# Kernel optimization log

Measured on AMD Instinct MI355X. Metric: run time of the kernel, lower is better.

The kernel has to match this reference:

```python
import jax, jax.numpy as jnp
import numpy as np

B = 4096   # batch (samples)
V = 64     # num_vars
H = 512    # hidden_dim


def setup_inputs() -> dict:
    key = jax.random.key(0)
    k0, k1, k2, k3 = jax.random.split(key, 4)
    x = jax.random.normal(k0, (B, V), dtype=jnp.float32)
    # learned params: adjacency logits + stacked per-variable 2-layer MLPs
    adj_weights = jax.random.normal(k1, (V, V), dtype=jnp.float32) * 0.1
    W1 = jax.random.normal(k2, (V, V - 1, H), dtype=jnp.float32) * (1.0 / np.sqrt(V - 1))
    b1 = jnp.zeros((V, H), dtype=jnp.float32)
    W2 = jax.random.normal(k3, (V, H), dtype=jnp.float32) * (1.0 / np.sqrt(H))
    b2 = jnp.zeros((V,), dtype=jnp.float32)
    return {"x": x, "adj_weights": adj_weights, "W1": W1, "b1": b1, "W2": W2, "b2": b2}


def reference(x, adj_weights, W1, b1, W2, b2):
    Vn = adj_weights.shape[0]
    # sigmoid adjacency with zeroed diagonal
    adj = jax.nn.sigmoid(adj_weights) * (1.0 - jnp.eye(Vn, dtype=adj_weights.dtype))
    # idx[i, j] = j if j < i else j + 1  -> columns of x excluding variable i
    j = jnp.arange(Vn - 1)
    idx = j[None, :] + (j[None, :] >= jnp.arange(Vn)[:, None])  # [V, V-1] int
    gathered = x[:, idx]                                  # [B, V, V-1]
    w = jnp.take_along_axis(adj, idx, axis=1)             # [V, V-1] (row i, cols != i)
    weighted = gathered * w[None, :, :]                   # [B, V, V-1]
    # batched small MLP per variable
    h = jax.nn.relu(jnp.einsum('bvk,vkh->bvh', weighted, W1) + b1[None])  # [B, V, H]
    out = jnp.einsum('bvh,vh->bv', h, W2) + b2[None]                      # [B, V]
    return out
```

## Files before the change

### kernel.cpp

```cpp
#include <hip/hip_runtime.h>
#include <hip/hip_bf16.h>

constexpr int Bn = 4096;
constexpr int Vn = 64;
constexpr int Hn = 512;

typedef __attribute__((ext_vector_type(8))) short bf16x8;
typedef __attribute__((ext_vector_type(4))) float f32x4;
typedef __attribute__((ext_vector_type(8))) unsigned short u16x8;
typedef __attribute__((ext_vector_type(4))) _Float16 f16x4;

__device__ __forceinline__ unsigned short f2bf(float f) {
    union { float f; unsigned int u; } x; x.f = f;
    unsigned int u = x.u;
    u += 0x7fffu + ((u >> 16) & 1u);
    return (unsigned short)(u >> 16);
}

__global__ void prep_all(const float* __restrict__ adjw,
                         const float* __restrict__ W1,
                         const float* __restrict__ x,
                         unsigned short* __restrict__ bfrag,
                         unsigned short* __restrict__ afrag) {
    if (blockIdx.x < 1024) {
        int nb   = (blockIdx.x & 7) * 128 + (blockIdx.x >> 3);
        int tid  = nb * 256 + threadIdx.x;
        int lane = tid & 63;
        int ks   = (tid >> 6) & 1;
        int nt   = (tid >> 7) & 31;
        int v    = tid >> 12;

        int n     = nt * 16 + (lane & 15);
        int kbase = ks * 32 + ((lane >> 4) << 3);

        u16x8 o;
#pragma unroll
        for (int e = 0; e < 8; ++e) {
            int k = kbase + e;
            float val = 0.f;
            if (k != v) {
                float aw = adjw[v * Vn + k];
                float s  = 1.f / (1.f + __expf(-aw));
                int  j   = k - (k > v);
                val = s * W1[((size_t)(v * (Vn - 1) + j)) * Hn + n];
            }
            o[e] = f2bf(val);
        }
        *reinterpret_cast<u16x8*>(bfrag + (size_t)tid * 8) = o;
    } else {
        int tid  = (blockIdx.x - 1024) * 256 + threadIdx.x;
        int lane = tid & 63;
        int ks   = (tid >> 6) & 1;
        int mt   = tid >> 7;

        int b     = mt * 16 + (lane & 15);
        int kbase = ks * 32 + ((lane >> 4) << 3);

        u16x8 o;
#pragma unroll
        for (int e = 0; e < 8; ++e)
            o[e] = f2bf(x[(size_t)b * Vn + kbase + e]);
        *reinterpret_cast<u16x8*>(afrag + (size_t)tid * 8) = o;
    }
}

__global__ __launch_bounds__(512, 4)
void main_k(const unsigned short* __restrict__ afrag,
            const unsigned short* __restrict__ bfrag,
            const float* __restrict__ b1, const float* __restrict__ W2,
            const float* __restrict__ b2, float* __restrict__ out) {
    __shared__ __align__(16) unsigned char smem[2 * 16384 + 512 * 9 * 4];

    int t    = threadIdx.x;
    int wid  = t >> 6;
    int lane = t & 63;
    int xcd  = blockIdx.x & 7;
    int idx  = blockIdx.x >> 3;
    int v    = xcd * 8 + (idx & 7);
    int ro   = idx >> 3;

    int hi4  = (lane >> 4) << 2;

    const unsigned short* wpan = bfrag + (size_t)v * 32768;
    bf16x8 Wf[4][2];
#pragma unroll
    for (int j = 0; j < 4; ++j)
#pragma unroll
        for (int ks = 0; ks < 2; ++ks)
            Wf[j][ks] = *reinterpret_cast<const bf16x8*>(
                wpan + ((size_t)((wid * 4 + j) * 2 + ks)) * 512 + lane * 8);

    f32x4 b1bc[4];
    f16x4 w2A[4];
#pragma unroll
    for (int j = 0; j < 4; ++j) {
        int ntg = wid * 4 + j;
        b1bc[j] = *reinterpret_cast<const f32x4*>(b1 + v * Hn + ntg * 16 + hi4);
        f32x4 wv = *reinterpret_cast<const f32x4*>(W2 + v * Hn + ntg * 16 + hi4);
#pragma unroll
        for (int e = 0; e < 4; ++e) w2A[j][e] = (_Float16)wv[e];
    }

    const unsigned char* asrc = reinterpret_cast<const unsigned char*>(afrag)
                              + (size_t)ro * 65536;
    {
        u16x8 s0 = *reinterpret_cast<const u16x8*>(asrc + t * 16);
        u16x8 s1 = *reinterpret_cast<const u16x8*>(asrc + 8192 + t * 16);
        *reinterpret_cast<u16x8*>(smem + t * 16) = s0;
        *reinterpret_cast<u16x8*>(smem + 8192 + t * 16) = s1;
    }
    __syncthreads();

    float* partials = reinterpret_cast<float*>(smem + 32768);

#pragma unroll
    for (int c = 0; c < 4; ++c) {
        u16x8 s0, s1;
        if (c < 3) {
            s0 = *reinterpret_cast<const u16x8*>(asrc + (c + 1) * 16384 + t * 16);
            s1 = *reinterpret_cast<const u16x8*>(asrc + (c + 1) * 16384 + 8192 + t * 16);
        }

        const unsigned char* lb = smem + (c & 1) * 16384;
#pragma unroll
        for (int mt = 0; mt < 8; ++mt) {
            bf16x8 a0 = *reinterpret_cast<const bf16x8*>(lb + ((mt * 2 + 0) * 64 + lane) * 16);
            bf16x8 a1 = *reinterpret_cast<const bf16x8*>(lb + ((mt * 2 + 1) * 64 + lane) * 16);
            f32x4 acc = {0.f, 0.f, 0.f, 0.f};
#pragma unroll
            for (int j = 0; j < 4; ++j) {
                f32x4 c1 = __builtin_amdgcn_mfma_f32_16x16x32_bf16(Wf[j][0], a0, b1bc[j], 0, 0, 0);
                c1 = __builtin_amdgcn_mfma_f32_16x16x32_bf16(Wf[j][1], a1, c1, 0, 0, 0);
                f16x4 hb;
#pragma unroll
                for (int e = 0; e < 4; ++e)
                    hb[e] = (_Float16)fmaxf(c1[e], 0.f);
                acc = __builtin_amdgcn_mfma_f32_16x16x16f16(w2A[j], hb, acc, 0, 0, 0);
            }
            if (lane < 16)
                partials[(c * 128 + mt * 16 + lane) * 9 + wid] = acc[0];
        }

        if (c < 3) {
            unsigned char* nbuf = smem + ((c + 1) & 1) * 16384;
            *reinterpret_cast<u16x8*>(nbuf + t * 16) = s0;
            *reinterpret_cast<u16x8*>(nbuf + 8192 + t * 16) = s1;
        }
        __syncthreads();
    }

    float s = b2[v];
#pragma unroll
    for (int w = 0; w < 8; ++w) s += partials[t * 9 + w];
    out[(size_t)(ro * 512 + t) * Vn + v] = s;
}

extern "C" void kernel_launch(void* const* d_in, const int* in_sizes, int n_in,
                              void* d_out, int out_size, void* d_ws, size_t ws_size,
                              hipStream_t stream) {
    const float* x    = (const float*)d_in[0];
    const float* adjw = (const float*)d_in[1];
    const float* W1   = (const float*)d_in[2];
    const float* b1   = (const float*)d_in[3];
    const float* W2   = (const float*)d_in[4];
    const float* b2   = (const float*)d_in[5];
    float* out = (float*)d_out;

    unsigned short* bfrag = (unsigned short*)d_ws;
    unsigned short* afrag = bfrag + (size_t)Vn * Vn * Hn;

    prep_all<<<1152, 256, 0, stream>>>(adjw, W1, x, bfrag, afrag);
    main_k<<<512, 512, 0, stream>>>(afrag, bfrag, b1, W2, b2, out);
}
```

Measured before the change: 30.22 us.

## Fuse weight and input bf16 prep into main kernel, drop prep launch

```diff
diff --git a/kernel.cpp b/kernel.cpp
--- a/kernel.cpp
+++ b/kernel.cpp
@@ -10,6 +10,8 @@
 typedef __attribute__((ext_vector_type(8))) unsigned short u16x8;
 typedef __attribute__((ext_vector_type(4))) _Float16 f16x4;
 
+union bfcast { u16x8 u; bf16x8 b; };
+
 __device__ __forceinline__ unsigned short f2bf(float f) {
     union { float f; unsigned int u; } x; x.f = f;
     unsigned int u = x.u;
@@ -17,79 +19,42 @@
     return (unsigned short)(u >> 16);
 }
 
-__global__ void prep_all(const float* __restrict__ adjw,
-                         const float* __restrict__ W1,
-                         const float* __restrict__ x,
-                         unsigned short* __restrict__ bfrag,
-                         unsigned short* __restrict__ afrag) {
-    if (blockIdx.x < 1024) {
-        int nb   = (blockIdx.x & 7) * 128 + (blockIdx.x >> 3);
-        int tid  = nb * 256 + threadIdx.x;
-        int lane = tid & 63;
-        int ks   = (tid >> 6) & 1;
-        int nt   = (tid >> 7) & 31;
-        int v    = tid >> 12;
-
-        int n     = nt * 16 + (lane & 15);
-        int kbase = ks * 32 + ((lane >> 4) << 3);
-
-        u16x8 o;
-#pragma unroll
-        for (int e = 0; e < 8; ++e) {
-            int k = kbase + e;
-            float val = 0.f;
-            if (k != v) {
-                float aw = adjw[v * Vn + k];
-                float s  = 1.f / (1.f + __expf(-aw));
-                int  j   = k - (k > v);
-                val = s * W1[((size_t)(v * (Vn - 1) + j)) * Hn + n];
-            }
-            o[e] = f2bf(val);
-        }
-        *reinterpret_cast<u16x8*>(bfrag + (size_t)tid * 8) = o;
-    } else {
-        int tid  = (blockIdx.x - 1024) * 256 + threadIdx.x;
-        int lane = tid & 63;
-        int ks   = (tid >> 6) & 1;
-        int mt   = tid >> 7;
-
-        int b     = mt * 16 + (lane & 15);
-        int kbase = ks * 32 + ((lane >> 4) << 3);
-
-        u16x8 o;
-#pragma unroll
-        for (int e = 0; e < 8; ++e)
-            o[e] = f2bf(x[(size_t)b * Vn + kbase + e]);
-        *reinterpret_cast<u16x8*>(afrag + (size_t)tid * 8) = o;
-    }
-}
-
 __global__ __launch_bounds__(512, 4)
-void main_k(const unsigned short* __restrict__ afrag,
-            const unsigned short* __restrict__ bfrag,
+void main_k(const float* __restrict__ x,
+            const float* __restrict__ adjw,
+            const float* __restrict__ W1,
             const float* __restrict__ b1, const float* __restrict__ W2,
             const float* __restrict__ b2, float* __restrict__ out) {
-    __shared__ __align__(16) unsigned char smem[2 * 16384 + 512 * 9 * 4];
+    __shared__ __align__(16) unsigned char smem[2 * 16384 + 512 * 9 * 4 + 256];
+    float* partials = reinterpret_cast<float*>(smem + 2 * 16384);
+    float* sig      = reinterpret_cast<float*>(smem + 2 * 16384 + 512 * 9 * 4);
 
     int t    = threadIdx.x;
     int wid  = t >> 6;
     int lane = t & 63;
-    int xcd  = blockIdx.x & 7;
-    int idx  = blockIdx.x >> 3;
-    int v    = xcd * 8 + (idx & 7);
-    int ro   = idx >> 3;
+    int v    = (blockIdx.x & 7) * 8 + ((blockIdx.x >> 3) & 7);
+    int ro   = blockIdx.x >> 6;
 
-    int hi4  = (lane >> 4) << 2;
+    if (t < 64) {
+        float aw = adjw[v * Vn + t];
+        sig[t] = (t == v) ? 0.f : 1.f / (1.f + __expf(-aw));
+    }
 
-    const unsigned short* wpan = bfrag + (size_t)v * 32768;
-    bf16x8 Wf[4][2];
-#pragma unroll
-    for (int j = 0; j < 4; ++j)
-#pragma unroll
-        for (int ks = 0; ks < 2; ++ks)
-            Wf[j][ks] = *reinterpret_cast<const bf16x8*>(
-                wpan + ((size_t)((wid * 4 + j) * 2 + ks)) * 512 + lane * 8);
+    int s_mt  = t >> 7;
+    int s_ks  = (t >> 6) & 1;
+    int s_kb  = s_ks * 32 + ((lane >> 4) << 3);
+    int r0    = s_mt * 16 + (lane & 15);
+    int r1    = (s_mt + 4) * 16 + (lane & 15);
+    const float* xb0 = x + ((size_t)(ro * 512 + r0)) * Vn + s_kb;
+    const float* xb1 = x + ((size_t)(ro * 512 + r1)) * Vn + s_kb;
+    f32x4 c0a = *reinterpret_cast<const f32x4*>(xb0);
+    f32x4 c0b = *reinterpret_cast<const f32x4*>(xb0 + 4);
+    f32x4 c0c = *reinterpret_cast<const f32x4*>(xb1);
+    f32x4 c0d = *reinterpret_cast<const f32x4*>(xb1 + 4);
 
+    __syncthreads();
+
+    int hi4 = (lane >> 4) << 2;
     f32x4 b1bc[4];
     f16x4 w2A[4];
 #pragma unroll
@@ -101,24 +66,47 @@
         for (int e = 0; e < 4; ++e) w2A[j][e] = (_Float16)wv[e];
     }
 
-    const unsigned char* asrc = reinterpret_cast<const unsigned char*>(afrag)
-                              + (size_t)ro * 65536;
+    bf16x8 Wf[4][2];
+#pragma unroll
+    for (int j = 0; j < 4; ++j)
+#pragma unroll
+        for (int ks = 0; ks < 2; ++ks) {
+            int n     = (wid * 4 + j) * 16 + (lane & 15);
+            int kbase = ks * 32 + ((lane >> 4) << 3);
+            bfcast tc;
+#pragma unroll
+            for (int e = 0; e < 8; ++e) {
+                int k = kbase + e;
+                float val = 0.f;
+                if (k != v)
+                    val = sig[k] * W1[((size_t)(v * (Vn - 1) + (k - (k > v)))) * Hn + n];
+                tc.u[e] = f2bf(val);
+            }
+            Wf[j][ks] = tc.b;
+        }
+
     {
-        u16x8 s0 = *reinterpret_cast<const u16x8*>(asrc + t * 16);
-        u16x8 s1 = *reinterpret_cast<const u16x8*>(asrc + 8192 + t * 16);
-        *reinterpret_cast<u16x8*>(smem + t * 16) = s0;
-        *reinterpret_cast<u16x8*>(smem + 8192 + t * 16) = s1;
+        bfcast t0, t1;
+#pragma unroll
+        for (int e = 0; e < 4; ++e) {
+            t0.u[e] = f2bf(c0a[e]);  t0.u[e + 4] = f2bf(c0b[e]);
+            t1.u[e] = f2bf(c0c[e]);  t1.u[e + 4] = f2bf(c0d[e]);
+        }
+        *reinterpret_cast<u16x8*>(smem + t * 16)         = t0.u;
+        *reinterpret_cast<u16x8*>(smem + (t + 512) * 16) = t1.u;
     }
     __syncthreads();
 
-    float* partials = reinterpret_cast<float*>(smem + 32768);
-
 #pragma unroll
     for (int c = 0; c < 4; ++c) {
-        u16x8 s0, s1;
+        f32x4 na, nb, nc, nd;
         if (c < 3) {
-            s0 = *reinterpret_cast<const u16x8*>(asrc + (c + 1) * 16384 + t * 16);
-            s1 = *reinterpret_cast<const u16x8*>(asrc + (c + 1) * 16384 + 8192 + t * 16);
+            const float* n0 = xb0 + (size_t)(c + 1) * 128 * Vn;
+            const float* n1 = xb1 + (size_t)(c + 1) * 128 * Vn;
+            na = *reinterpret_cast<const f32x4*>(n0);
+            nb = *reinterpret_cast<const f32x4*>(n0 + 4);
+            nc = *reinterpret_cast<const f32x4*>(n1);
+            nd = *reinterpret_cast<const f32x4*>(n1 + 4);
         }
 
         const unsigned char* lb = smem + (c & 1) * 16384;
@@ -143,8 +131,14 @@
 
         if (c < 3) {
             unsigned char* nbuf = smem + ((c + 1) & 1) * 16384;
-            *reinterpret_cast<u16x8*>(nbuf + t * 16) = s0;
-            *reinterpret_cast<u16x8*>(nbuf + 8192 + t * 16) = s1;
+            bfcast t0, t1;
+#pragma unroll
+            for (int e = 0; e < 4; ++e) {
+                t0.u[e] = f2bf(na[e]);  t0.u[e + 4] = f2bf(nb[e]);
+                t1.u[e] = f2bf(nc[e]);  t1.u[e + 4] = f2bf(nd[e]);
+            }
+            *reinterpret_cast<u16x8*>(nbuf + t * 16)         = t0.u;
+            *reinterpret_cast<u16x8*>(nbuf + (t + 512) * 16) = t1.u;
         }
         __syncthreads();
     }
@@ -166,9 +160,5 @@
     const float* b2   = (const float*)d_in[5];
     float* out = (float*)d_out;
 
-    unsigned short* bfrag = (unsigned short*)d_ws;
-    unsigned short* afrag = bfrag + (size_t)Vn * Vn * Hn;
-
-    prep_all<<<1152, 256, 0, stream>>>(adjw, W1, x, bfrag, afrag);
-    main_k<<<512, 512, 0, stream>>>(afrag, bfrag, b1, W2, b2, out);
+    main_k<<<512, 512, 0, stream>>>(x, adjw, W1, b1, W2, b2, out);
 }
```

After: 44.01 us. 1.46x slower.

## Halve per-block batch rows, double grid, split MFMA accumulators, use pkrtz conversion

Applied to the files above, without the earlier changes.

```diff
diff --git a/kernel.cpp b/kernel.cpp
--- a/kernel.cpp
+++ b/kernel.cpp
@@ -9,6 +9,10 @@
 typedef __attribute__((ext_vector_type(4))) float f32x4;
 typedef __attribute__((ext_vector_type(8))) unsigned short u16x8;
 typedef __attribute__((ext_vector_type(4))) _Float16 f16x4;
+typedef __attribute__((ext_vector_type(2))) __fp16 fp16v2;
+
+union bfcast { u16x8 u; bf16x8 b; };
+union h4cast { fp16v2 h2[2]; f16x4 f4; };
 
 __device__ __forceinline__ unsigned short f2bf(float f) {
     union { float f; unsigned int u; } x; x.f = f;
@@ -69,17 +73,17 @@
             const unsigned short* __restrict__ bfrag,
             const float* __restrict__ b1, const float* __restrict__ W2,
             const float* __restrict__ b2, float* __restrict__ out) {
-    __shared__ __align__(16) unsigned char smem[2 * 16384 + 512 * 9 * 4];
+    __shared__ __align__(16) unsigned char smem[2 * 8192 + 256 * 9 * 4];
+    float* partials = reinterpret_cast<float*>(smem + 2 * 8192);
 
     int t    = threadIdx.x;
     int wid  = t >> 6;
     int lane = t & 63;
-    int xcd  = blockIdx.x & 7;
-    int idx  = blockIdx.x >> 3;
-    int v    = xcd * 8 + (idx & 7);
-    int ro   = idx >> 3;
+    int v    = (blockIdx.x & 7) * 8 + ((blockIdx.x >> 3) & 7);
+    int ro   = blockIdx.x >> 6;
 
-    int hi4  = (lane >> 4) << 2;
+    const u16x8* asrc = reinterpret_cast<const u16x8*>(afrag) + (size_t)ro * 2048;
+    u16x8 s0 = asrc[t];
 
     const unsigned short* wpan = bfrag + (size_t)v * 32768;
     bf16x8 Wf[4][2];
@@ -90,6 +94,7 @@
             Wf[j][ks] = *reinterpret_cast<const bf16x8*>(
                 wpan + ((size_t)((wid * 4 + j) * 2 + ks)) * 512 + lane * 8);
 
+    int hi4 = (lane >> 4) << 2;
     f32x4 b1bc[4];
     f16x4 w2A[4];
 #pragma unroll
@@ -101,58 +106,54 @@
         for (int e = 0; e < 4; ++e) w2A[j][e] = (_Float16)wv[e];
     }
 
-    const unsigned char* asrc = reinterpret_cast<const unsigned char*>(afrag)
-                              + (size_t)ro * 65536;
-    {
-        u16x8 s0 = *reinterpret_cast<const u16x8*>(asrc + t * 16);
-        u16x8 s1 = *reinterpret_cast<const u16x8*>(asrc + 8192 + t * 16);
-        *reinterpret_cast<u16x8*>(smem + t * 16) = s0;
-        *reinterpret_cast<u16x8*>(smem + 8192 + t * 16) = s1;
-    }
+    *reinterpret_cast<u16x8*>(smem + t * 16) = s0;
     __syncthreads();
-
-    float* partials = reinterpret_cast<float*>(smem + 32768);
 
 #pragma unroll
     for (int c = 0; c < 4; ++c) {
-        u16x8 s0, s1;
-        if (c < 3) {
-            s0 = *reinterpret_cast<const u16x8*>(asrc + (c + 1) * 16384 + t * 16);
-            s1 = *reinterpret_cast<const u16x8*>(asrc + (c + 1) * 16384 + 8192 + t * 16);
-        }
+        u16x8 sn;
+        if (c < 3) sn = asrc[(c + 1) * 512 + t];
 
-        const unsigned char* lb = smem + (c & 1) * 16384;
+        const unsigned char* lb = smem + (c & 1) * 8192;
 #pragma unroll
-        for (int mt = 0; mt < 8; ++mt) {
+        for (int mt = 0; mt < 4; ++mt) {
             bf16x8 a0 = *reinterpret_cast<const bf16x8*>(lb + ((mt * 2 + 0) * 64 + lane) * 16);
             bf16x8 a1 = *reinterpret_cast<const bf16x8*>(lb + ((mt * 2 + 1) * 64 + lane) * 16);
-            f32x4 acc = {0.f, 0.f, 0.f, 0.f};
+            f32x4 accA = {0.f, 0.f, 0.f, 0.f};
+            f32x4 accB = {0.f, 0.f, 0.f, 0.f};
 #pragma unroll
-            for (int j = 0; j < 4; ++j) {
-                f32x4 c1 = __builtin_amdgcn_mfma_f32_16x16x32_bf16(Wf[j][0], a0, b1bc[j], 0, 0, 0);
-                c1 = __builtin_amdgcn_mfma_f32_16x16x32_bf16(Wf[j][1], a1, c1, 0, 0, 0);
-                f16x4 hb;
+            for (int p = 0; p < 2; ++p) {
 #pragma unroll
-                for (int e = 0; e < 4; ++e)
-                    hb[e] = (_Float16)fmaxf(c1[e], 0.f);
-                acc = __builtin_amdgcn_mfma_f32_16x16x16f16(w2A[j], hb, acc, 0, 0, 0);
+                for (int q = 0; q < 2; ++q) {
+                    int j = 2 * p + q;
+                    f32x4 c1 = __builtin_amdgcn_mfma_f32_16x16x32_bf16(Wf[j][0], a0, b1bc[j], 0, 0, 0);
+                    c1 = __builtin_amdgcn_mfma_f32_16x16x32_bf16(Wf[j][1], a1, c1, 0, 0, 0);
+                    h4cast hc;
+                    hc.h2[0] = __builtin_amdgcn_cvt_pkrtz(fmaxf(c1[0], 0.f), fmaxf(c1[1], 0.f));
+                    hc.h2[1] = __builtin_amdgcn_cvt_pkrtz(fmaxf(c1[2], 0.f), fmaxf(c1[3], 0.f));
+                    if (q == 0)
+                        accA = __builtin_amdgcn_mfma_f32_16x16x16f16(w2A[j], hc.f4, accA, 0, 0, 0);
+                    else
+                        accB = __builtin_amdgcn_mfma_f32_16x16x16f16(w2A[j], hc.f4, accB, 0, 0, 0);
+                }
             }
             if (lane < 16)
-                partials[(c * 128 + mt * 16 + lane) * 9 + wid] = acc[0];
+                partials[(c * 64 + mt * 16 + lane) * 9 + wid] = accA[0] + accB[0];
         }
 
         if (c < 3) {
-            unsigned char* nbuf = smem + ((c + 1) & 1) * 16384;
-            *reinterpret_cast<u16x8*>(nbuf + t * 16) = s0;
-            *reinterpret_cast<u16x8*>(nbuf + 8192 + t * 16) = s1;
+            unsigned char* nbuf = smem + ((c + 1) & 1) * 8192;
+            *reinterpret_cast<u16x8*>(nbuf + t * 16) = sn;
         }
         __syncthreads();
     }
 
-    float s = b2[v];
+    if (t < 256) {
+        float s = b2[v];
 #pragma unroll
-    for (int w = 0; w < 8; ++w) s += partials[t * 9 + w];
-    out[(size_t)(ro * 512 + t) * Vn + v] = s;
+        for (int w = 0; w < 8; ++w) s += partials[t * 9 + w];
+        out[(size_t)(ro * 256 + t) * Vn + v] = s;
+    }
 }
 
 extern "C" void kernel_launch(void* const* d_in, const int* in_sizes, int n_in,
@@ -170,5 +171,5 @@
     unsigned short* afrag = bfrag + (size_t)Vn * Vn * Hn;
 
     prep_all<<<1152, 256, 0, stream>>>(adjw, W1, x, bfrag, afrag);
-    main_k<<<512, 512, 0, stream>>>(afrag, bfrag, b1, W2, b2, out);
+    main_k<<<1024, 512, 0, stream>>>(afrag, bfrag, b1, W2, b2, out);
 }
```

After: 30.74 us. No clear change (+1.7%).
